# Kernel tuning notes

Measured on AMD Instinct MI355X. Metric: run time of the kernel, lower is better.

The kernel has to match this reference:

```python
import jax, jax.numpy as jnp
import numpy as np

N_EL = 4            # allowed elements (H, C, N, O)
N_EXPERTS = N_EL * N_EL
F_ATOM = 176        # per-atom symmetry feature dim
F_PAIR = 32         # pair feature dim (2*F_ATOM + F_PAIR == 384 == nodes[0])


def _init_linear(key, fin, fout, n):
    # torch nn.Linear default init: U(-1/sqrt(fin), 1/sqrt(fin))
    bound = 1.0 / np.sqrt(fin)
    kw, kb = jax.random.split(key)
    W = jax.random.uniform(kw, (n, fin, fout), minval=-bound, maxval=bound, dtype=jnp.float32)
    b = jax.random.uniform(kb, (n, fout), minval=-bound, maxval=bound, dtype=jnp.float32)
    return W, b


def setup_inputs() -> dict:
    key = jax.random.key(0)
    ks = jax.random.split(key, 8)
    B, A, C = 128, 128, 256
    elements = jax.random.randint(ks[0], (B, A), 0, N_EL)
    connectivity = jax.random.randint(ks[1], (B, C, 2), 0, A)
    sym_features = jax.random.normal(ks[2], (B, A, F_ATOM), dtype=jnp.float32)
    pair_features = jax.random.normal(ks[3], (B, C, F_PAIR), dtype=jnp.float32)
    W1, b1 = _init_linear(ks[4], 384, 128, N_EXPERTS)
    W2, b2 = _init_linear(ks[5], 128, 96, N_EXPERTS)
    W3, b3 = _init_linear(ks[6], 96, 2, N_EXPERTS)
    return dict(elements=elements, connectivity=connectivity,
                sym_features=sym_features, pair_features=pair_features,
                W1=W1, b1=b1, W2=W2, b2=b2, W3=W3, b3=b3)


def _pair_moe(elements, connectivity, sym_features, pair_features, W1, b1, W2, b2, W3, b3):
    B, C, _ = connectivity.shape
    A = sym_features.shape[1]
    out_dim = W3.shape[-1]

    # mirror: mask padded pairs (connectivity[...,0] == -1) before offsetting
    mask = (connectivity[..., 0] != -1).reshape(-1)              # [B*C]
    conn_f = (connectivity + (jnp.arange(B) * A)[:, None, None]).reshape(-1, 2)
    idx0 = jnp.where(mask, conn_f[:, 0], 0)
    idx1 = jnp.where(mask, conn_f[:, 1], 0)

    feat_f = sym_features.reshape(-1, sym_features.shape[-1])    # [B*A, F]
    el_f = elements.reshape(-1)                                  # [B*A]

    m = mask[:, None].astype(sym_features.dtype)
    fa = feat_f[idx0] * m                                        # [B*C, F] (zeros where padded)
    fb = feat_f[idx1] * m
    e0 = jnp.where(mask, el_f[idx0], -1)
    e1 = jnp.where(mask, el_f[idx1], -1)
    nn_index = e0 * N_EL + e1                                    # -5 for padded pairs -> no expert

    x = jnp.concatenate([fa, fb, pair_features.reshape(-1, pair_features.shape[-1])], axis=1)

    y = jnp.zeros((x.shape[0], out_dim), dtype=x.dtype)
    for i in range(N_EXPERTS):  # fixed small expert set (structural loop)
        h = jax.nn.celu(x @ W1[i] + b1[i])
        h = jax.nn.celu(h @ W2[i] + b2[i])
        o = h @ W3[i] + b3[i]
        y = jnp.where((nn_index == i)[:, None], o, y)
    return y.reshape(B, C, out_dim)


def reference(elements, connectivity, sym_features, pair_features, W1, b1, W2, b2, W3, b3):
    # Original returns (elements, connectivity, y); only y is computed output.
    return _pair_moe(elements, connectivity, sym_features, pair_features, W1, b1, W2, b2, W3, b3)
```

## Files before the change

### kernel.cpp

```cpp
#include <hip/hip_runtime.h>
#include <math.h>

typedef __attribute__((ext_vector_type(8))) short short8;
typedef __attribute__((ext_vector_type(4))) float f32x4;

namespace {
constexpr int NEL   = 4;
constexpr int NEXP  = 16;
constexpr int Bb    = 128;
constexpr int Aa    = 128;
constexpr int Cc    = 256;
constexpr int FATOM = 176;
constexpr int FPAIR = 32;
constexpr int FIN   = 384;
constexpr int HH1   = 128;
constexpr int HH2   = 96;
constexpr int NP    = Bb * Cc;
constexpr int NA    = Bb * Aa;
constexpr int BUCKET_CAP = 4096;

constexpr int WS_COUNTS = 0;
constexpr int WS_B2     = 64;
constexpr int WS_SHORTS = 64 + NEXP * BUCKET_CAP * 4;

constexpr int W2_OFF = 12 * HH1 * 32;
constexpr int WPK_E  = W2_OFF + 4 * HH2 * 32;
constexpr int WPK_N  = NEXP * WPK_E;

constexpr int SYM_N  = NA * FATOM;
constexpr int PAIR_N = NP * FPAIR;

constexpr int CVT_BLOCKS = (SYM_N / 4 + PAIR_N / 4) / 256;
constexpr int W1_BLOCKS  = 768;
constexpr int W2_BLOCKS  = 192;
constexpr int IDX_BLOCKS = NP / 256;
constexpr int W1_BASE  = CVT_BLOCKS;
constexpr int W2_BASE  = W1_BASE + W1_BLOCKS;
constexpr int IDX_BASE = W2_BASE + W2_BLOCKS;
constexpr int PREP_GRID = IDX_BASE + IDX_BLOCKS;
}

__device__ inline short f2bf(float f) {
    unsigned u = __builtin_bit_cast(unsigned, f);
    unsigned r = (u + 0x7FFFu + ((u >> 16) & 1u)) >> 16;
    return (short)r;
}
__device__ inline float celu1(float v) {
    return v > 0.f ? v : (__expf(v) - 1.0f);
}

__global__ __launch_bounds__(256) void k_prep(
    const float* __restrict__ sym, const float* __restrict__ pairf,
    short* __restrict__ symb, short* __restrict__ pairfb,
    const float* __restrict__ W1, const float* __restrict__ W2,
    short* __restrict__ wpk,
    const int* __restrict__ conn, const int* __restrict__ elements,
    int* __restrict__ counts, int4* __restrict__ bucket2,
    float* __restrict__ out)
{
    __shared__ float T[32][33];
    __shared__ int sh_cnt[NEXP], sh_base[NEXP];

    int bid = blockIdx.x;
    int t = threadIdx.x;

    if (bid < CVT_BLOCKS) {
        int i = bid * 256 + t;
        constexpr int NS4 = SYM_N / 4;
        const float4* src; short* dst; int j;
        if (i < NS4) { src = (const float4*)sym;   dst = symb;   j = i; }
        else         { src = (const float4*)pairf; dst = pairfb; j = i - NS4; }
        float4 v = src[j];
        short4 o;
        o.x = f2bf(v.x); o.y = f2bf(v.y); o.z = f2bf(v.z); o.w = f2bf(v.w);
        *(short4*)(dst + 4 * (size_t)j) = o;
    } else if (bid < IDX_BASE) {
        const float* src; short* dst; int N, k0, n0;
        if (bid < W2_BASE) {
            int b1i = bid - W1_BASE;
            int e = b1i / 48, tl = b1i % 48;
            N = HH1; k0 = (tl % 12) * 32; n0 = (tl / 12) * 32;
            src = W1 + (size_t)e * FIN * HH1;
            dst = wpk + (size_t)e * WPK_E;
        } else {
            int b2i = bid - W2_BASE;
            int e = b2i / 12, tl = b2i % 12;
            N = HH2; k0 = (tl % 4) * 32; n0 = (tl / 4) * 32;
            src = W2 + (size_t)e * HH1 * HH2;
            dst = wpk + (size_t)e * WPK_E + W2_OFF;
        }
        int tx = t & 31, ty = t >> 5;
        int ks = k0 >> 5;
#pragma unroll
        for (int j = 0; j < 4; ++j) {
            int r = ty + 8 * j;
            T[r][tx] = src[(size_t)(k0 + r) * N + n0 + tx];
        }
        __syncthreads();
#pragma unroll
        for (int j = 0; j < 4; ++j) {
            int n = n0 + ty + 8 * j;
            dst[(size_t)(ks * N + n) * 32 + tx] = f2bf(T[tx][ty + 8 * j]);
        }
    } else {
        int p = (bid - IDX_BASE) * 256 + t;
        if (t < NEXP) sh_cnt[t] = 0;
        __syncthreads();
        int e = -1, r = 0, i0 = 0, i1 = 0;
        {
            int c0 = conn[2 * p], c1 = conn[2 * p + 1];
            if (c0 != -1) {
                int b = p / Cc;
                i0 = b * Aa + c0; if (i0 < 0) i0 += NA;
                i1 = b * Aa + c1; if (i1 < 0) i1 += NA;
                e = elements[i0] * NEL + elements[i1];
            }
            if (e < 0 || e >= NEXP) {
                out[2 * p] = 0.f; out[2 * p + 1] = 0.f;
                e = -1;
            } else {
                r = atomicAdd(&sh_cnt[e], 1);
            }
        }
        __syncthreads();
        if (t < NEXP) sh_base[t] = (sh_cnt[t] > 0) ? atomicAdd(&counts[t], sh_cnt[t]) : 0;
        __syncthreads();
        if (e >= 0) {
            int pos = sh_base[e] + r;
            if (pos < BUCKET_CAP) {
                int4 rec; rec.x = p; rec.y = i0; rec.z = i1; rec.w = 0;
                bucket2[e * BUCKET_CAP + pos] = rec;
            }
        }
    }
}

#define GATHER2(A, REC) do {                                                  \
    const short* fa = symb + (size_t)((REC).y & (NA - 1)) * FATOM;            \
    const short* fb = symb + (size_t)((REC).z & (NA - 1)) * FATOM;            \
    const short* pf = pairfb + (size_t)((REC).x & (NP - 1)) * FPAIR;          \
    A[0]  = *(const short8*)(fa + 8 * lg);                                    \
    A[1]  = *(const short8*)(fa + 32 + 8 * lg);                               \
    A[2]  = *(const short8*)(fa + 64 + 8 * lg);                               \
    A[3]  = *(const short8*)(fa + 96 + 8 * lg);                               \
    A[4]  = *(const short8*)(fa + 128 + 8 * lg);                              \
    A[5]  = *(const short8*)((lg < 2 ? fa + 160 : fb - 16) + 8 * lg);         \
    A[6]  = *(const short8*)(fb + 16 + 8 * lg);                               \
    A[7]  = *(const short8*)(fb + 48 + 8 * lg);                               \
    A[8]  = *(const short8*)(fb + 80 + 8 * lg);                               \
    A[9]  = *(const short8*)(fb + 112 + 8 * lg);                              \
    A[10] = *(const short8*)(fb + 144 + 8 * lg);                              \
    A[11] = *(const short8*)(pf + 8 * lg);                                    \
} while (0)

__global__ __launch_bounds__(512, 2) void k_moe(
    const int* __restrict__ counts, const int4* __restrict__ bucket2,
    const short* __restrict__ symb, const short* __restrict__ pairfb,
    const short* __restrict__ wpk,
    const float* __restrict__ b1, const float* __restrict__ b2,
    const float* __restrict__ W3, const float* __restrict__ b3,
    float* __restrict__ out)
{
    __shared__ short Wlds[WPK_E];
    __shared__ short H1s[8][16 * HH1];

    int e     = blockIdx.x & 15;
    int shard = blockIdx.x >> 4;
    int cnt = counts[e];
    if (cnt > BUCKET_CAP) cnt = BUCKET_CAP;
    int nt = (cnt + 31) >> 5;

    int t = threadIdx.x;
    int w = t >> 6;
    int lane = t & 63;
    int lr = lane & 15, lg = (lane >> 4) & 3;

    const int4* b2e = bucket2 + e * BUCKET_CAP;
    const short* wsrc = wpk + (size_t)e * WPK_E;

    int tile = w * 16 + shard;
    bool active = tile < nt;

    int ii0 = tile * 32 + lr;
    int ii1 = ii0 + 16;
    int cm1 = cnt > 0 ? cnt - 1 : 0;
    int4 rec0 = b2e[active ? (ii0 < cnt ? ii0 : cm1) : 0];
    int4 rec1 = b2e[active ? (ii1 < cnt ? ii1 : cm1) : 0];
    short8 aA[12], aB[12];
    GATHER2(aA, rec0);
    GATHER2(aB, rec1);
    __builtin_amdgcn_sched_barrier(0);

    short8 v[15];
#pragma unroll
    for (int r = 0; r < 15; ++r) v[r] = *(const short8*)(wsrc + r * 4096 + t * 8);
    float b1v[8];
#pragma unroll
    for (int j = 0; j < 8; ++j) b1v[j] = b1[e * HH1 + j * 16 + lr];
    float2 b3v = ((const float2*)b3)[e];
    __builtin_amdgcn_sched_barrier(0);

#pragma unroll
    for (int r = 0; r < 15; ++r) *(short8*)&Wlds[r * 4096 + t * 8] = v[r];
    __syncthreads();

    if (!active) return;

    short* h1w = &H1s[w][0];

    f32x4 acc[2][8];
#pragma unroll
    for (int j = 0; j < 8; ++j) {
        acc[0][j] = (f32x4){b1v[j], b1v[j], b1v[j], b1v[j]};
        acc[1][j] = acc[0][j];
    }
#pragma unroll
    for (int ks = 0; ks < 12; ++ks) {
#pragma unroll
        for (int j = 0; j < 8; ++j) {
            short8 bw = *(const short8*)&Wlds[(ks * HH1 + j * 16 + lr) * 32 + 8 * lg];
            acc[0][j] = __builtin_amdgcn_mfma_f32_16x16x32_bf16(aA[ks], bw, acc[0][j], 0, 0, 0);
            acc[1][j] = __builtin_amdgcn_mfma_f32_16x16x32_bf16(aB[ks], bw, acc[1][j], 0, 0, 0);
        }
    }

#pragma unroll
    for (int mi = 0; mi < 2; ++mi) {
#pragma unroll
        for (int j = 0; j < 8; ++j)
#pragma unroll
            for (int r2 = 0; r2 < 4; ++r2) {
                int m = 4 * lg + r2;
                int n = 16 * j + lr;
                h1w[m * HH1 + (((n >> 3) ^ (m & 7)) << 3) + (n & 7)] = f2bf(celu1(acc[mi][j][r2]));
            }
        asm volatile("s_waitcnt lgkmcnt(0)" ::: "memory");
        __builtin_amdgcn_sched_barrier(0);

        int mx = lr & 7;
        short8 bh0 = *(const short8*)&h1w[lr * HH1 + (((0 + lg) ^ mx) << 3)];
        short8 bh1 = *(const short8*)&h1w[lr * HH1 + (((4 + lg) ^ mx) << 3)];
        short8 bh2 = *(const short8*)&h1w[lr * HH1 + (((8 + lg) ^ mx) << 3)];
        short8 bh3 = *(const short8*)&h1w[lr * HH1 + (((12 + lg) ^ mx) << 3)];

        float s0 = 0.f, s1 = 0.f;
#pragma unroll
        for (int t6 = 0; t6 < 6; ++t6) {
            int n2b = 16 * t6 + 4 * lg;
            float4 bb4 = *(const float4*)&b2[e * HH2 + n2b];
            f32x4 a2c;
            a2c[0] = bb4.x; a2c[1] = bb4.y; a2c[2] = bb4.z; a2c[3] = bb4.w;
            {
                short8 aw = *(const short8*)&Wlds[W2_OFF + (0 * HH2 + 16 * t6 + lr) * 32 + 8 * lg];
                a2c = __builtin_amdgcn_mfma_f32_16x16x32_bf16(aw, bh0, a2c, 0, 0, 0);
            }
            {
                short8 aw = *(const short8*)&Wlds[W2_OFF + (1 * HH2 + 16 * t6 + lr) * 32 + 8 * lg];
                a2c = __builtin_amdgcn_mfma_f32_16x16x32_bf16(aw, bh1, a2c, 0, 0, 0);
            }
            {
                short8 aw = *(const short8*)&Wlds[W2_OFF + (2 * HH2 + 16 * t6 + lr) * 32 + 8 * lg];
                a2c = __builtin_amdgcn_mfma_f32_16x16x32_bf16(aw, bh2, a2c, 0, 0, 0);
            }
            {
                short8 aw = *(const short8*)&Wlds[W2_OFF + (3 * HH2 + 16 * t6 + lr) * 32 + 8 * lg];
                a2c = __builtin_amdgcn_mfma_f32_16x16x32_bf16(aw, bh3, a2c, 0, 0, 0);
            }
            float4 w3a = *(const float4*)&W3[(size_t)(e * HH2 + n2b) * 2];
            float4 w3b = *(const float4*)&W3[(size_t)(e * HH2 + n2b) * 2 + 4];
            float h0 = celu1(a2c[0]), h1c = celu1(a2c[1]), h2 = celu1(a2c[2]), h3 = celu1(a2c[3]);
            s0 = fmaf(h0, w3a.x, fmaf(h1c, w3a.z, fmaf(h2, w3b.x, fmaf(h3, w3b.z, s0))));
            s1 = fmaf(h0, w3a.y, fmaf(h1c, w3a.w, fmaf(h2, w3b.y, fmaf(h3, w3b.w, s1))));
        }
        s0 += __shfl_xor(s0, 16); s0 += __shfl_xor(s0, 32);
        s1 += __shfl_xor(s1, 16); s1 += __shfl_xor(s1, 32);
        int ii = mi == 0 ? ii0 : ii1;
        int pp = (mi == 0 ? rec0.x : rec1.x) & (NP - 1);
        if (((lane >> 4) & 3) == 0 && ii < cnt) {
            float2 o2; o2.x = s0 + b3v.x; o2.y = s1 + b3v.y;
            *(float2*)(out + 2 * (size_t)pp) = o2;
        }
    }
}

extern "C" void kernel_launch(void* const* d_in, const int* in_sizes, int n_in,
                              void* d_out, int out_size, void* d_ws, size_t ws_size,
                              hipStream_t stream)
{
    const int*   elements = (const int*)d_in[0];
    const int*   conn     = (const int*)d_in[1];
    const float* sym      = (const float*)d_in[2];
    const float* pairf    = (const float*)d_in[3];
    const float* W1       = (const float*)d_in[4];
    const float* b1       = (const float*)d_in[5];
    const float* W2       = (const float*)d_in[6];
    const float* b2       = (const float*)d_in[7];
    const float* W3       = (const float*)d_in[8];
    const float* b3       = (const float*)d_in[9];
    float* out = (float*)d_out;

    int* wsi     = (int*)d_ws;
    int* counts  = wsi + WS_COUNTS;
    int4* bucket2 = (int4*)(wsi + WS_B2);

    short* sbase  = (short*)(wsi + WS_SHORTS);
    short* wpk    = sbase;
    short* symb   = sbase + WPK_N;
    short* pairfb = sbase + WPK_N + SYM_N;

    hipMemsetAsync((void*)counts, 0, NEXP * sizeof(int), stream);

    k_prep<<<PREP_GRID, 256, 0, stream>>>(sym, pairf, symb, pairfb,
                                          W1, W2, wpk,
                                          conn, elements, counts, bucket2, out);
    k_moe<<<256, 512, 0, stream>>>(counts, bucket2, symb, pairfb, wpk,
                                   b1, b2, W3, b3, out);
}
```

Measured before the change: 32.02 us.

## Load expert weights directly to LDS and prefetch A fragments one k-step ahead

Weight staging into LDS now uses global_load_lds direct-to-LDS copies instead of going through registers, freeing 15 short8 registers per thread. The 24 register-held A fragments for the first GEMM are replaced by a rolled k-loop that prefetches the next k-step's gather while the current MFMAs run. This cuts register pressure and may raise occupancy, but it exposes gather latency inside the loop, where a single step of prefetch may not hide it.

```diff
diff --git a/kernel.cpp b/kernel.cpp
--- a/kernel.cpp
+++ b/kernel.cpp
@@ -47,6 +47,11 @@
 }
 __device__ inline float celu1(float v) {
     return v > 0.f ? v : (__expf(v) - 1.0f);
+}
+__device__ inline void gl_lds16(const short* g, short* l) {
+    __builtin_amdgcn_global_load_lds(
+        (const __attribute__((address_space(1))) void*)g,
+        (__attribute__((address_space(3))) void*)l, 16, 0, 0);
 }
 
 __global__ __launch_bounds__(256) void k_prep(
@@ -135,22 +140,58 @@
     }
 }
 
-#define GATHER2(A, REC) do {                                                  \
-    const short* fa = symb + (size_t)((REC).y & (NA - 1)) * FATOM;            \
-    const short* fb = symb + (size_t)((REC).z & (NA - 1)) * FATOM;            \
-    const short* pf = pairfb + (size_t)((REC).x & (NP - 1)) * FPAIR;          \
-    A[0]  = *(const short8*)(fa + 8 * lg);                                    \
-    A[1]  = *(const short8*)(fa + 32 + 8 * lg);                               \
-    A[2]  = *(const short8*)(fa + 64 + 8 * lg);                               \
-    A[3]  = *(const short8*)(fa + 96 + 8 * lg);                               \
-    A[4]  = *(const short8*)(fa + 128 + 8 * lg);                              \
-    A[5]  = *(const short8*)((lg < 2 ? fa + 160 : fb - 16) + 8 * lg);         \
-    A[6]  = *(const short8*)(fb + 16 + 8 * lg);                               \
-    A[7]  = *(const short8*)(fb + 48 + 8 * lg);                               \
-    A[8]  = *(const short8*)(fb + 80 + 8 * lg);                               \
-    A[9]  = *(const short8*)(fb + 112 + 8 * lg);                              \
-    A[10] = *(const short8*)(fb + 144 + 8 * lg);                              \
-    A[11] = *(const short8*)(pf + 8 * lg);                                    \
+__device__ inline const short* aptr(int ks, const short* fa, const short* fb,
+                                    const short* pf, int lg)
+{
+    if (ks < 5)  return fa + 32 * ks + 8 * lg;
+    if (ks == 5) return (lg < 2 ? fa + 160 : fb - 16) + 8 * lg;
+    if (ks < 11) return fb + 16 + 32 * (ks - 6) + 8 * lg;
+    return pf + 8 * lg;
+}
+
+#define EPILOG(ACC, II, PP) do {                                              \
+    _Pragma("unroll")                                                         \
+    for (int j = 0; j < 8; ++j)                                               \
+        _Pragma("unroll")                                                     \
+        for (int r2 = 0; r2 < 4; ++r2) {                                      \
+            int m = 4 * lg + r2;                                              \
+            int n = 16 * j + lr;                                              \
+            h1w[m * HH1 + (((n >> 3) ^ (m & 7)) << 3) + (n & 7)] = f2bf(celu1(ACC[j][r2])); \
+        }                                                                     \
+    asm volatile("s_waitcnt lgkmcnt(0)" ::: "memory");                        \
+    __builtin_amdgcn_sched_barrier(0);                                        \
+    int mx = lr & 7;                                                          \
+    short8 bh0 = *(const short8*)&h1w[lr * HH1 + (((0 + lg) ^ mx) << 3)];     \
+    short8 bh1 = *(const short8*)&h1w[lr * HH1 + (((4 + lg) ^ mx) << 3)];     \
+    short8 bh2 = *(const short8*)&h1w[lr * HH1 + (((8 + lg) ^ mx) << 3)];     \
+    short8 bh3 = *(const short8*)&h1w[lr * HH1 + (((12 + lg) ^ mx) << 3)];    \
+    float s0 = 0.f, s1 = 0.f;                                                 \
+    _Pragma("unroll")                                                         \
+    for (int t6 = 0; t6 < 6; ++t6) {                                          \
+        int n2b = 16 * t6 + 4 * lg;                                           \
+        float4 bb4 = *(const float4*)&b2[e * HH2 + n2b];                      \
+        f32x4 a2c;                                                            \
+        a2c[0] = bb4.x; a2c[1] = bb4.y; a2c[2] = bb4.z; a2c[3] = bb4.w;       \
+        short8 aw0 = *(const short8*)&Wlds[W2_OFF + (0 * HH2 + 16 * t6 + lr) * 32 + 8 * lg]; \
+        a2c = __builtin_amdgcn_mfma_f32_16x16x32_bf16(aw0, bh0, a2c, 0, 0, 0); \
+        short8 aw1 = *(const short8*)&Wlds[W2_OFF + (1 * HH2 + 16 * t6 + lr) * 32 + 8 * lg]; \
+        a2c = __builtin_amdgcn_mfma_f32_16x16x32_bf16(aw1, bh1, a2c, 0, 0, 0); \
+        short8 aw2 = *(const short8*)&Wlds[W2_OFF + (2 * HH2 + 16 * t6 + lr) * 32 + 8 * lg]; \
+        a2c = __builtin_amdgcn_mfma_f32_16x16x32_bf16(aw2, bh2, a2c, 0, 0, 0); \
+        short8 aw3 = *(const short8*)&Wlds[W2_OFF + (3 * HH2 + 16 * t6 + lr) * 32 + 8 * lg]; \
+        a2c = __builtin_amdgcn_mfma_f32_16x16x32_bf16(aw3, bh3, a2c, 0, 0, 0); \
+        float4 w3a = *(const float4*)&W3[(size_t)(e * HH2 + n2b) * 2];        \
+        float4 w3b = *(const float4*)&W3[(size_t)(e * HH2 + n2b) * 2 + 4];    \
+        float h0 = celu1(a2c[0]), h1c = celu1(a2c[1]), h2 = celu1(a2c[2]), h3 = celu1(a2c[3]); \
+        s0 = fmaf(h0, w3a.x, fmaf(h1c, w3a.z, fmaf(h2, w3b.x, fmaf(h3, w3b.z, s0)))); \
+        s1 = fmaf(h0, w3a.y, fmaf(h1c, w3a.w, fmaf(h2, w3b.y, fmaf(h3, w3b.w, s1)))); \
+    }                                                                         \
+    s0 += __shfl_xor(s0, 16); s0 += __shfl_xor(s0, 32);                       \
+    s1 += __shfl_xor(s1, 16); s1 += __shfl_xor(s1, 32);                       \
+    if (((lane >> 4) & 3) == 0 && (II) < cnt) {                               \
+        float2 o2; o2.x = s0 + b3v.x; o2.y = s1 + b3v.y;                      \
+        *(float2*)(out + 2 * (size_t)(PP)) = o2;                              \
+    }                                                                         \
 } while (0)
 
 __global__ __launch_bounds__(512, 2) void k_moe(
@@ -161,8 +202,8 @@
     const float* __restrict__ W3, const float* __restrict__ b3,
     float* __restrict__ out)
 {
-    __shared__ short Wlds[WPK_E];
-    __shared__ short H1s[8][16 * HH1];
+    __shared__ __align__(16) short Wlds[WPK_E];
+    __shared__ __align__(16) short H1s[8][16 * HH1];
 
     int e     = blockIdx.x & 15;
     int shard = blockIdx.x >> 4;
@@ -186,101 +227,55 @@
     int cm1 = cnt > 0 ? cnt - 1 : 0;
     int4 rec0 = b2e[active ? (ii0 < cnt ? ii0 : cm1) : 0];
     int4 rec1 = b2e[active ? (ii1 < cnt ? ii1 : cm1) : 0];
-    short8 aA[12], aB[12];
-    GATHER2(aA, rec0);
-    GATHER2(aB, rec1);
-    __builtin_amdgcn_sched_barrier(0);
-
-    short8 v[15];
-#pragma unroll
-    for (int r = 0; r < 15; ++r) v[r] = *(const short8*)(wsrc + r * 4096 + t * 8);
+
+#pragma unroll
+    for (int r = 0; r < 15; ++r)
+        gl_lds16(wsrc + r * 4096 + t * 8, &Wlds[r * 4096 + t * 8]);
+
     float b1v[8];
 #pragma unroll
     for (int j = 0; j < 8; ++j) b1v[j] = b1[e * HH1 + j * 16 + lr];
     float2 b3v = ((const float2*)b3)[e];
-    __builtin_amdgcn_sched_barrier(0);
-
-#pragma unroll
-    for (int r = 0; r < 15; ++r) *(short8*)&Wlds[r * 4096 + t * 8] = v[r];
+
+    const short* faA = symb + (size_t)(rec0.y & (NA - 1)) * FATOM;
+    const short* fbA = symb + (size_t)(rec0.z & (NA - 1)) * FATOM;
+    const short* pfA = pairfb + (size_t)(rec0.x & (NP - 1)) * FPAIR;
+    const short* faB = symb + (size_t)(rec1.y & (NA - 1)) * FATOM;
+    const short* fbB = symb + (size_t)(rec1.z & (NA - 1)) * FATOM;
+    const short* pfB = pairfb + (size_t)(rec1.x & (NP - 1)) * FPAIR;
+    short8 aAc = *(const short8*)aptr(0, faA, fbA, pfA, lg);
+    short8 aBc = *(const short8*)aptr(0, faB, fbB, pfB, lg);
+
     __syncthreads();
-
     if (!active) return;
 
     short* h1w = &H1s[w][0];
 
-    f32x4 acc[2][8];
+    f32x4 acc0[8], acc1[8];
 #pragma unroll
     for (int j = 0; j < 8; ++j) {
-        acc[0][j] = (f32x4){b1v[j], b1v[j], b1v[j], b1v[j]};
-        acc[1][j] = acc[0][j];
+        acc0[j] = (f32x4){b1v[j], b1v[j], b1v[j], b1v[j]};
+        acc1[j] = acc0[j];
     }
-#pragma unroll
+#pragma unroll 1
     for (int ks = 0; ks < 12; ++ks) {
+        int ksn = ks < 11 ? ks + 1 : 11;
+        short8 aAn = *(const short8*)aptr(ksn, faA, fbA, pfA, lg);
+        short8 aBn = *(const short8*)aptr(ksn, faB, fbB, pfB, lg);
+        const short* wbase = &Wlds[(ks * HH1 + lr) * 32 + 8 * lg];
 #pragma unroll
         for (int j = 0; j < 8; ++j) {
-            short8 bw = *(const short8*)&Wlds[(ks * HH1 + j * 16 + lr) * 32 + 8 * lg];
-            acc[0][j] = __builtin_amdgcn_mfma_f32_16x16x32_bf16(aA[ks], bw, acc[0][j], 0, 0, 0);
-            acc[1][j] = __builtin_amdgcn_mfma_f32_16x16x32_bf16(aB[ks], bw, acc[1][j], 0, 0, 0);
-        }
+            short8 bw = *(const short8*)(wbase + j * 16 * 32);
+            acc0[j] = __builtin_amdgcn_mfma_f32_16x16x32_bf16(aAc, bw, acc0[j], 0, 0, 0);
+            acc1[j] = __builtin_amdgcn_mfma_f32_16x16x32_bf16(aBc, bw, acc1[j], 0, 0, 0);
+        }
+        aAc = aAn; aBc = aBn;
     }
 
-#pragma unroll
-    for (int mi = 0; mi < 2; ++mi) {
-#pragma unroll
-        for (int j = 0; j < 8; ++j)
-#pragma unroll
-            for (int r2 = 0; r2 < 4; ++r2) {
-                int m = 4 * lg + r2;
-                int n = 16 * j + lr;
-                h1w[m * HH1 + (((n >> 3) ^ (m & 7)) << 3) + (n & 7)] = f2bf(celu1(acc[mi][j][r2]));
-            }
-        asm volatile("s_waitcnt lgkmcnt(0)" ::: "memory");
-        __builtin_amdgcn_sched_barrier(0);
-
-        int mx = lr & 7;
-        short8 bh0 = *(const short8*)&h1w[lr * HH1 + (((0 + lg) ^ mx) << 3)];
-        short8 bh1 = *(const short8*)&h1w[lr * HH1 + (((4 + lg) ^ mx) << 3)];
-        short8 bh2 = *(const short8*)&h1w[lr * HH1 + (((8 + lg) ^ mx) << 3)];
-        short8 bh3 = *(const short8*)&h1w[lr * HH1 + (((12 + lg) ^ mx) << 3)];
-
-        float s0 = 0.f, s1 = 0.f;
-#pragma unroll
-        for (int t6 = 0; t6 < 6; ++t6) {
-            int n2b = 16 * t6 + 4 * lg;
-            float4 bb4 = *(const float4*)&b2[e * HH2 + n2b];
-            f32x4 a2c;
-            a2c[0] = bb4.x; a2c[1] = bb4.y; a2c[2] = bb4.z; a2c[3] = bb4.w;
-            {
-                short8 aw = *(const short8*)&Wlds[W2_OFF + (0 * HH2 + 16 * t6 + lr) * 32 + 8 * lg];
-                a2c = __builtin_amdgcn_mfma_f32_16x16x32_bf16(aw, bh0, a2c, 0, 0, 0);
-            }
-            {
-                short8 aw = *(const short8*)&Wlds[W2_OFF + (1 * HH2 + 16 * t6 + lr) * 32 + 8 * lg];
-                a2c = __builtin_amdgcn_mfma_f32_16x16x32_bf16(aw, bh1, a2c, 0, 0, 0);
-            }
-            {
-                short8 aw = *(const short8*)&Wlds[W2_OFF + (2 * HH2 + 16 * t6 + lr) * 32 + 8 * lg];
-                a2c = __builtin_amdgcn_mfma_f32_16x16x32_bf16(aw, bh2, a2c, 0, 0, 0);
-            }
-            {
-                short8 aw = *(const short8*)&Wlds[W2_OFF + (3 * HH2 + 16 * t6 + lr) * 32 + 8 * lg];
-                a2c = __builtin_amdgcn_mfma_f32_16x16x32_bf16(aw, bh3, a2c, 0, 0, 0);
-            }
-            float4 w3a = *(const float4*)&W3[(size_t)(e * HH2 + n2b) * 2];
-            float4 w3b = *(const float4*)&W3[(size_t)(e * HH2 + n2b) * 2 + 4];
-            float h0 = celu1(a2c[0]), h1c = celu1(a2c[1]), h2 = celu1(a2c[2]), h3 = celu1(a2c[3]);
-            s0 = fmaf(h0, w3a.x, fmaf(h1c, w3a.z, fmaf(h2, w3b.x, fmaf(h3, w3b.z, s0))));
-            s1 = fmaf(h0, w3a.y, fmaf(h1c, w3a.w, fmaf(h2, w3b.y, fmaf(h3, w3b.w, s1))));
-        }
-        s0 += __shfl_xor(s0, 16); s0 += __shfl_xor(s0, 32);
-        s1 += __shfl_xor(s1, 16); s1 += __shfl_xor(s1, 32);
-        int ii = mi == 0 ? ii0 : ii1;
-        int pp = (mi == 0 ? rec0.x : rec1.x) & (NP - 1);
-        if (((lane >> 4) & 3) == 0 && ii < cnt) {
-            float2 o2; o2.x = s0 + b3v.x; o2.y = s1 + b3v.y;
-            *(float2*)(out + 2 * (size_t)pp) = o2;
-        }
-    }
+    int pp0 = rec0.x & (NP - 1);
+    int pp1 = rec1.x & (NP - 1);
+    EPILOG(acc0, ii0, pp0);
+    EPILOG(acc1, ii1, pp1);
 }
 
 extern "C" void kernel_launch(void* const* d_in, const int* in_sizes, int n_in,
```

Result: slower. 34.26 us (+7.0%).
